# Kernel optimization log

Hardware: AMD Instinct MI355X
Metric: run time of the kernel (lower is better)

The kernel has to match this reference:

```python
import jax, jax.numpy as jnp
import numpy as np

SEQ, B, D = 2048, 16, 1024  # seq_len, batch, input/hidden size

def setup_inputs() -> dict:
    key = jax.random.key(0)
    k1, k2, k3 = jax.random.split(key, 3)
    X = jax.random.normal(k1, (SEQ, B, D), dtype=jnp.float32)
    hidden = jnp.zeros((B, D), dtype=jnp.float32)  # initial hidden state C_0
    # nn.Linear(window*input_size, 3*hidden_size): weight (3D, D), bias (3D,)
    W = jax.random.normal(k2, (3 * D, D), dtype=jnp.float32) / np.float32(np.sqrt(D))
    b = jax.random.normal(k3, (3 * D,), dtype=jnp.float32) * 0.01
    return {"X": X, "hidden": hidden, "W": W, "b": b}

def _forget_mult(F, Z, h0):
    # C_t = F_t * Z_t + (1 - F_t) * C_{t-1}, scanned over seq dim
    def step(h, fz):
        f, z = fz
        h = f * z + (1.0 - f) * h
        return h, h
    _, C = jax.lax.scan(step, h0, (F, Z))
    return C  # (S, B, D)

def reference(X, hidden, W, b):
    # window=1 -> source = X; gate projection
    Y = jnp.einsum('sbd,hd->sbh', X, W) + b        # (S, B, 3D)
    Z, F, O = jnp.split(Y, 3, axis=2)
    Z = jnp.tanh(Z)
    F = jax.nn.sigmoid(F)
    C = _forget_mult(F, Z, hidden)                 # (S, B, D)
    H = jax.nn.sigmoid(O) * C                      # output gate (QRNN-fo)
    return H, C[-1:]                               # (S,B,D), (1,B,D)
```

## Files before the change

kernel.cpp:

```cpp
#include <hip/hip_runtime.h>


#define S_LEN 2048
#define BATCH 16
#define DHID 1024
#define N3 3072
#define MROWS (S_LEN * BATCH)
#define XELEMS ((size_t)MROWS * DHID)
#define WELEMS ((size_t)N3 * DHID)
#define YELEMS ((size_t)MROWS * N3)

typedef __attribute__((ext_vector_type(8))) short bf16x8;
typedef __attribute__((ext_vector_type(4))) float floatx4;
typedef __attribute__((ext_vector_type(4))) unsigned short u16x4;

__device__ __forceinline__ float b2f(unsigned short u) {
  return __uint_as_float(((unsigned)u) << 16);
}
__device__ __forceinline__ unsigned short f2b(float x) {
  unsigned u = __float_as_uint(x);
  u += 0x7fffu + ((u >> 16) & 1u);
  return (unsigned short)(u >> 16);
}
__device__ __forceinline__ float sigmoid_f(float x) {
  return __builtin_amdgcn_rcpf(1.0f + __expf(-x));
}
__device__ __forceinline__ float tanh_f(float x) {
  return 2.0f * __builtin_amdgcn_rcpf(1.0f + __expf(-2.0f * x)) - 1.0f;
}

__device__ __forceinline__ void load_lds16(const unsigned short* g, unsigned short* l) {
  __builtin_amdgcn_global_load_lds(
      (const __attribute__((address_space(1))) void*)g,
      (__attribute__((address_space(3))) void*)l,
      16, 0, 0);
}

__global__ __launch_bounds__(256) void cvt_f32_bf16(
    const float* __restrict__ src, unsigned short* __restrict__ dst, int n4) {
  int i = blockIdx.x * 256 + threadIdx.x;
  if (i < n4) {
    float4 v = ((const float4*)src)[i];
    u16x4 o;
    o.x = f2b(v.x); o.y = f2b(v.y); o.z = f2b(v.z); o.w = f2b(v.w);
    ((u16x4*)dst)[i] = o;
  }
}

__global__ __launch_bounds__(256) void qrnn_gemm(
    const unsigned short* __restrict__ X,
    const unsigned short* __restrict__ W,
    const float* __restrict__ bias,
    unsigned short* __restrict__ Y)
{
  __shared__ __align__(16) unsigned short sA[128 * 64];
  __shared__ __align__(16) unsigned short sB[128 * 64];

  const int tid = threadIdx.x;
  const int w  = tid >> 6;
  const int l  = tid & 63;
  const int lr = l & 15;
  const int lq = l >> 4;
  const int n0B = blockIdx.x * 128;
  const int m0B = blockIdx.y * 128;
  const int wm = (w >> 1) * 64;
  const int wn = (w & 1) * 64;

  floatx4 acc[4][4] = {};

  const unsigned short* gA = X + (size_t)m0B * DHID;
  const unsigned short* gB = W + (size_t)n0B * DHID;
  const int srow = tid >> 3;
  const int scol = (tid & 7) << 3;

  for (int k0 = 0; k0 < DHID; k0 += 64) {
#pragma unroll
    for (int j = 0; j < 4; ++j) {
      load_lds16(gA + (size_t)(j * 32 + srow) * DHID + (k0 + scol),
                 sA + (j * 2048 + w * 512));
      load_lds16(gB + (size_t)(j * 32 + srow) * DHID + (k0 + scol),
                 sB + (j * 2048 + w * 512));
    }
    __syncthreads();

#pragma unroll
    for (int kk = 0; kk < 64; kk += 32) {
      bf16x8 af[4], bf[4];
#pragma unroll
      for (int i = 0; i < 4; ++i) {
        af[i] = *(const bf16x8*)&sA[(wm + i * 16 + lr) * 64 + kk + lq * 8];
      }
#pragma unroll
      for (int j = 0; j < 4; ++j) {
        bf[j] = *(const bf16x8*)&sB[(wn + j * 16 + lr) * 64 + kk + lq * 8];
      }
#pragma unroll
      for (int i = 0; i < 4; ++i) {
#pragma unroll
        for (int j = 0; j < 4; ++j) {
          acc[i][j] = __builtin_amdgcn_mfma_f32_16x16x32_bf16(
              af[i], bf[j], acc[i][j], 0, 0, 0);
        }
      }
    }
    __syncthreads();
  }

  const int seg = n0B >> 10;
#pragma unroll
  for (int j = 0; j < 4; ++j) {
    const int n = n0B + wn + j * 16 + lr;
    const float bv = bias[n];
#pragma unroll
    for (int i = 0; i < 4; ++i) {
      const int mb = m0B + wm + i * 16 + lq * 4;
#pragma unroll
      for (int r = 0; r < 4; ++r) {
        float v = acc[i][j][r] + bv;
        v = (seg == 0) ? tanh_f(v) : sigmoid_f(v);
        Y[(size_t)(mb + r) * N3 + n] = f2b(v);
      }
    }
  }
}

#define U 8
#define PCH 16
#define LCH (S_LEN / PCH)
#define SUBCH (LCH / U)
#define SSTRIDE (BATCH * N3)
#define HSTRIDE (BATCH * DHID)
#define NT (BATCH * DHID)

__global__ __launch_bounds__(256) void qrnn_scan_pass1(
    const unsigned short* __restrict__ Y,
    float* __restrict__ Aarr,
    float* __restrict__ Barr)
{
  const int g = blockIdx.x * 256 + threadIdx.x;
  const int t = g & (NT - 1);
  const int p = g >> 14;
  const int b = t >> 10;
  const int d = t & 1023;
  const unsigned short* base =
      Y + (size_t)(p * LCH) * SSTRIDE + (size_t)b * N3 + d;

  float a = 1.0f, bv = 0.0f;
  unsigned short z0[U], f0[U], z1[U], f1[U];

#define LOADZF(ch, zz, ff) { \
    const unsigned short* p_ = base + (size_t)(ch) * ((size_t)U * SSTRIDE); \
    _Pragma("unroll") \
    for (int j2 = 0; j2 < U; ++j2) { \
      zz[j2] = p_[(size_t)j2 * SSTRIDE]; \
      ff[j2] = p_[(size_t)j2 * SSTRIDE + DHID]; \
    } }

#define COMPAB(zz, ff) { \
    _Pragma("unroll") \
    for (int j2 = 0; j2 < U; ++j2) { \
      float zv = b2f(zz[j2]); \
      float fv = b2f(ff[j2]); \
      a  = fmaf(-fv, a, a);             \
      bv = fmaf(fv, zv - bv, bv);       \
    } }

  LOADZF(0, z0, f0);
  for (int ch = 0; ch < SUBCH; ch += 2) {
    LOADZF(ch + 1, z1, f1);
    COMPAB(z0, f0);
    if (ch + 2 < SUBCH) LOADZF(ch + 2, z0, f0);
    COMPAB(z1, f1);
  }
  Aarr[g] = a;
  Barr[g] = bv;
}

__global__ __launch_bounds__(256) void qrnn_combine(
    const float* __restrict__ Aarr,
    const float* __restrict__ Barr,
    const float* __restrict__ h0,
    float* __restrict__ Cin,
    float* __restrict__ out)
{
  const int t = blockIdx.x * 256 + threadIdx.x;
  float c = h0[t];
#pragma unroll
  for (int p = 0; p < PCH; ++p) {
    Cin[p * NT + t] = c;
    c = fmaf(Aarr[p * NT + t], c, Barr[p * NT + t]);
  }
  out[(size_t)S_LEN * HSTRIDE + t] = c;
}

__global__ __launch_bounds__(256) void qrnn_scan_pass2(
    const unsigned short* __restrict__ Y,
    const float* __restrict__ Cin,
    float* __restrict__ out)
{
  const int g = blockIdx.x * 256 + threadIdx.x;
  const int t = g & (NT - 1);
  const int p = g >> 14;
  const int b = t >> 10;
  const int d = t & 1023;
  const unsigned short* base =
      Y + (size_t)(p * LCH) * SSTRIDE + (size_t)b * N3 + d;
  float* ho = out + (size_t)(p * LCH) * HSTRIDE + (size_t)b * DHID + d;
  float c = Cin[g];

  unsigned short z0[U], f0[U], o0[U], z1[U], f1[U], o1[U];

#define LOADCH(ch, zz, ff, oo) { \
    const unsigned short* p_ = base + (size_t)(ch) * ((size_t)U * SSTRIDE); \
    _Pragma("unroll") \
    for (int j2 = 0; j2 < U; ++j2) { \
      zz[j2] = p_[(size_t)j2 * SSTRIDE]; \
      ff[j2] = p_[(size_t)j2 * SSTRIDE + DHID]; \
      oo[j2] = p_[(size_t)j2 * SSTRIDE + 2 * DHID]; \
    } }

#define COMPCH(ch, zz, ff, oo) { \
    float* q = ho + (size_t)(ch) * ((size_t)U * HSTRIDE); \
    _Pragma("unroll") \
    for (int j2 = 0; j2 < U; ++j2) { \
      float zv = b2f(zz[j2]); \
      float fv = b2f(ff[j2]); \
      float ov = b2f(oo[j2]); \
      c = fmaf(fv, zv - c, c); \
      q[(size_t)j2 * HSTRIDE] = ov * c; \
    } }

  LOADCH(0, z0, f0, o0);
  for (int ch = 0; ch < SUBCH; ch += 2) {
    LOADCH(ch + 1, z1, f1, o1);
    COMPCH(ch, z0, f0, o0);
    if (ch + 2 < SUBCH) LOADCH(ch + 2, z0, f0, o0);
    COMPCH(ch + 1, z1, f1, o1);
  }
}

extern "C" void kernel_launch(void* const* d_in, const int* in_sizes, int n_in,
                              void* d_out, int out_size, void* d_ws, size_t ws_size,
                              hipStream_t stream) {
  const float* X    = (const float*)d_in[0];
  const float* h0   = (const float*)d_in[1];
  const float* W    = (const float*)d_in[2];
  const float* bias = (const float*)d_in[3];
  float* out = (float*)d_out;

  unsigned short* Ybf = (unsigned short*)d_ws;
  unsigned short* Wbf = Ybf + YELEMS;
  unsigned short* Xbf = (unsigned short*)out;
  float* Aarr = (float*)Wbf;
  float* Barr = Aarr + PCH * NT;
  float* CinA = Barr + PCH * NT;

  cvt_f32_bf16<<<(int)(XELEMS / 4 + 255) / 256, 256, 0, stream>>>(X, Xbf, (int)(XELEMS / 4));
  cvt_f32_bf16<<<(int)(WELEMS / 4 + 255) / 256, 256, 0, stream>>>(W, Wbf, (int)(WELEMS / 4));
  qrnn_gemm<<<dim3(N3 / 128, MROWS / 128), 256, 0, stream>>>(Xbf, Wbf, bias, Ybf);
  qrnn_scan_pass1<<<dim3((PCH * NT) / 256), 256, 0, stream>>>(Ybf, Aarr, Barr);
  qrnn_combine<<<dim3(NT / 256), 256, 0, stream>>>(Aarr, Barr, h0, CinA, out);
  qrnn_scan_pass2<<<dim3((PCH * NT) / 256), 256, 0, stream>>>(Ybf, CinA, out);
}
```

Baseline: 563.5 us.

## Store gate outputs in chain-major time-contiguous layout for vectorized scan loads

The GEMM epilogue now writes the activated Z/F/O gates into planes of 16 timesteps per chain, packing four timesteps into one 8-byte store. Each scan thread can then read 16 consecutive timesteps with 16-byte vector loads instead of strided 2-byte loads. The number of parallel chunks is doubled to 32, and the A/B arrays are relocated to the tail of the output buffer. The trade-offs are less coalesced stores in the GEMM epilogue and more carry-combine work.

```diff
diff --git a/kernel.cpp b/kernel.cpp
--- a/kernel.cpp
+++ b/kernel.cpp
@@ -106,29 +106,33 @@
     __syncthreads();
   }
 
-  const int seg = n0B >> 10;
+  const int gate = n0B >> 10;
+  const int srow_base = (m0B + wm) >> 4;
+  const int sblk = srow_base >> 4;
+  const int sin0 = srow_base & 15;
+  const size_t plane = (size_t)(sblk * 3 + gate) << 18;
 #pragma unroll
   for (int j = 0; j < 4; ++j) {
     const int n = n0B + wn + j * 16 + lr;
     const float bv = bias[n];
-#pragma unroll
-    for (int i = 0; i < 4; ++i) {
-      const int mb = m0B + wm + i * 16 + lq * 4;
-#pragma unroll
-      for (int r = 0; r < 4; ++r) {
+    const int dcol = n & 1023;
+#pragma unroll
+    for (int r = 0; r < 4; ++r) {
+      const int chain = ((lq * 4 + r) << 10) | dcol;
+      u16x4 pk;
+#pragma unroll
+      for (int i = 0; i < 4; ++i) {
         float v = acc[i][j][r] + bv;
-        v = (seg == 0) ? tanh_f(v) : sigmoid_f(v);
-        Y[(size_t)(mb + r) * N3 + n] = f2b(v);
-      }
-    }
-  }
-}
-
-#define U 8
-#define PCH 16
+        v = (gate == 0) ? tanh_f(v) : sigmoid_f(v);
+        pk[i] = f2b(v);
+      }
+      *(u16x4*)&Y[plane + ((size_t)chain << 4) + sin0] = pk;
+    }
+  }
+}
+
+#define PCH 32
 #define LCH (S_LEN / PCH)
-#define SUBCH (LCH / U)
-#define SSTRIDE (BATCH * N3)
 #define HSTRIDE (BATCH * DHID)
 #define NT (BATCH * DHID)
 
@@ -138,39 +142,32 @@
     float* __restrict__ Barr)
 {
   const int g = blockIdx.x * 256 + threadIdx.x;
-  const int t = g & (NT - 1);
+  const int c = g & (NT - 1);
   const int p = g >> 14;
-  const int b = t >> 10;
-  const int d = t & 1023;
-  const unsigned short* base =
-      Y + (size_t)(p * LCH) * SSTRIDE + (size_t)b * N3 + d;
+  const size_t cb = (size_t)c << 4;
 
   float a = 1.0f, bv = 0.0f;
-  unsigned short z0[U], f0[U], z1[U], f1[U];
-
-#define LOADZF(ch, zz, ff) { \
-    const unsigned short* p_ = base + (size_t)(ch) * ((size_t)U * SSTRIDE); \
-    _Pragma("unroll") \
-    for (int j2 = 0; j2 < U; ++j2) { \
-      zz[j2] = p_[(size_t)j2 * SSTRIDE]; \
-      ff[j2] = p_[(size_t)j2 * SSTRIDE + DHID]; \
-    } }
-
-#define COMPAB(zz, ff) { \
-    _Pragma("unroll") \
-    for (int j2 = 0; j2 < U; ++j2) { \
-      float zv = b2f(zz[j2]); \
-      float fv = b2f(ff[j2]); \
-      a  = fmaf(-fv, a, a);             \
-      bv = fmaf(fv, zv - bv, bv);       \
-    } }
-
-  LOADZF(0, z0, f0);
-  for (int ch = 0; ch < SUBCH; ch += 2) {
-    LOADZF(ch + 1, z1, f1);
-    COMPAB(z0, f0);
-    if (ch + 2 < SUBCH) LOADZF(ch + 2, z0, f0);
-    COMPAB(z1, f1);
+#pragma unroll
+  for (int gi = 0; gi < 4; ++gi) {
+    const size_t pl = ((size_t)((p * 4 + gi) * 3) << 18) + cb;
+    bf16x8 z0 = *(const bf16x8*)&Y[pl];
+    bf16x8 z1 = *(const bf16x8*)&Y[pl + 8];
+    bf16x8 f0 = *(const bf16x8*)&Y[pl + (1 << 18)];
+    bf16x8 f1 = *(const bf16x8*)&Y[pl + (1 << 18) + 8];
+#pragma unroll
+    for (int j = 0; j < 8; ++j) {
+      float zv = b2f((unsigned short)z0[j]);
+      float fv = b2f((unsigned short)f0[j]);
+      a  = fmaf(-fv, a, a);
+      bv = fmaf(fv, zv - bv, bv);
+    }
+#pragma unroll
+    for (int j = 0; j < 8; ++j) {
+      float zv = b2f((unsigned short)z1[j]);
+      float fv = b2f((unsigned short)f1[j]);
+      a  = fmaf(-fv, a, a);
+      bv = fmaf(fv, zv - bv, bv);
+    }
   }
   Aarr[g] = a;
   Barr[g] = bv;
@@ -199,43 +196,38 @@
     float* __restrict__ out)
 {
   const int g = blockIdx.x * 256 + threadIdx.x;
-  const int t = g & (NT - 1);
+  const int c = g & (NT - 1);
   const int p = g >> 14;
-  const int b = t >> 10;
-  const int d = t & 1023;
-  const unsigned short* base =
-      Y + (size_t)(p * LCH) * SSTRIDE + (size_t)b * N3 + d;
-  float* ho = out + (size_t)(p * LCH) * HSTRIDE + (size_t)b * DHID + d;
-  float c = Cin[g];
-
-  unsigned short z0[U], f0[U], o0[U], z1[U], f1[U], o1[U];
-
-#define LOADCH(ch, zz, ff, oo) { \
-    const unsigned short* p_ = base + (size_t)(ch) * ((size_t)U * SSTRIDE); \
-    _Pragma("unroll") \
-    for (int j2 = 0; j2 < U; ++j2) { \
-      zz[j2] = p_[(size_t)j2 * SSTRIDE]; \
-      ff[j2] = p_[(size_t)j2 * SSTRIDE + DHID]; \
-      oo[j2] = p_[(size_t)j2 * SSTRIDE + 2 * DHID]; \
-    } }
-
-#define COMPCH(ch, zz, ff, oo) { \
-    float* q = ho + (size_t)(ch) * ((size_t)U * HSTRIDE); \
-    _Pragma("unroll") \
-    for (int j2 = 0; j2 < U; ++j2) { \
-      float zv = b2f(zz[j2]); \
-      float fv = b2f(ff[j2]); \
-      float ov = b2f(oo[j2]); \
-      c = fmaf(fv, zv - c, c); \
-      q[(size_t)j2 * HSTRIDE] = ov * c; \
-    } }
-
-  LOADCH(0, z0, f0, o0);
-  for (int ch = 0; ch < SUBCH; ch += 2) {
-    LOADCH(ch + 1, z1, f1, o1);
-    COMPCH(ch, z0, f0, o0);
-    if (ch + 2 < SUBCH) LOADCH(ch + 2, z0, f0, o0);
-    COMPCH(ch + 1, z1, f1, o1);
+  const size_t cb = (size_t)c << 4;
+  float cst = Cin[g];
+  float* hb = out + c;
+
+#pragma unroll
+  for (int gi = 0; gi < 4; ++gi) {
+    const size_t pl = ((size_t)((p * 4 + gi) * 3) << 18) + cb;
+    bf16x8 z0 = *(const bf16x8*)&Y[pl];
+    bf16x8 z1 = *(const bf16x8*)&Y[pl + 8];
+    bf16x8 f0 = *(const bf16x8*)&Y[pl + (1 << 18)];
+    bf16x8 f1 = *(const bf16x8*)&Y[pl + (1 << 18) + 8];
+    bf16x8 o0 = *(const bf16x8*)&Y[pl + (2 << 18)];
+    bf16x8 o1 = *(const bf16x8*)&Y[pl + (2 << 18) + 8];
+    const int s0 = p * LCH + gi * 16;
+#pragma unroll
+    for (int j = 0; j < 8; ++j) {
+      float zv = b2f((unsigned short)z0[j]);
+      float fv = b2f((unsigned short)f0[j]);
+      float ov = b2f((unsigned short)o0[j]);
+      cst = fmaf(fv, zv - cst, cst);
+      hb[(size_t)(s0 + j) << 14] = ov * cst;
+    }
+#pragma unroll
+    for (int j = 0; j < 8; ++j) {
+      float zv = b2f((unsigned short)z1[j]);
+      float fv = b2f((unsigned short)f1[j]);
+      float ov = b2f((unsigned short)o1[j]);
+      cst = fmaf(fv, zv - cst, cst);
+      hb[(size_t)(s0 + 8 + j) << 14] = ov * cst;
+    }
   }
 }
 
@@ -251,9 +243,13 @@
   unsigned short* Ybf = (unsigned short*)d_ws;
   unsigned short* Wbf = Ybf + YELEMS;
   unsigned short* Xbf = (unsigned short*)out;
-  float* Aarr = (float*)Wbf;
-  float* Barr = Aarr + PCH * NT;
-  float* CinA = Barr + PCH * NT;
+  float* Aarr = out + ((size_t)S_LEN * HSTRIDE - 2 * (size_t)PCH * NT);
+  float* Barr = Aarr + (size_t)PCH * NT;
+  float* CinA = (float*)Wbf;
+  static_assert((size_t)PCH * NT * 4 <= (size_t)WELEMS * 2,
+                "Cin must fit in Wbf region");
+  static_assert(2 * (size_t)PCH * NT * 4 <= (size_t)64 * 1024 * 1024,
+                "A/B tail must stay clear of Xbf half");
 
   cvt_f32_bf16<<<(int)(XELEMS / 4 + 255) / 256, 256, 0, stream>>>(X, Xbf, (int)(XELEMS / 4));
   cvt_f32_bf16<<<(int)(WELEMS / 4 + 255) / 256, 256, 0, stream>>>(W, Wbf, (int)(WELEMS / 4));
```

New measurement: 628.8 us. +11.6%, slower.
